# Kernel optimization log

Hardware: AMD Instinct MI355X
Metric: run time of the kernel (lower is better)

## Reference

```python
import jax, jax.numpy as jnp
import numpy as np

NS, NW, E, DIN, OUT, H = 100_000, 400_000, 500_000, 64, 64, 4


def setup_inputs() -> dict:
    key = jax.random.key(0)
    ks = jax.random.split(key, 26)
    s = 1.0 / np.sqrt(DIN)
    sg = 1.0 / np.sqrt(OUT)
    inp = {
        "x_sites": jax.random.normal(ks[0], (NS, DIN), jnp.float32),
        "x_wells": jax.random.normal(ks[1], (NW, DIN), jnp.float32),
        "edge_sw_src": jax.random.randint(ks[2], (E,), 0, NS, jnp.int32),
        "edge_sw_dst": jax.random.randint(ks[3], (E,), 0, NW, jnp.int32),
        "edge_ws_src": jax.random.randint(ks[4], (E,), 0, NW, jnp.int32),
        "edge_ws_dst": jax.random.randint(ks[5], (E,), 0, NS, jnp.int32),
        # GAT ('pfas_sites','distance','gw_wells'), heads=4, concat=False
        "W_sw": jax.random.normal(ks[6], (DIN, H * OUT), jnp.float32) * s,
        "att_src_sw": jax.random.normal(ks[7], (H, OUT), jnp.float32) * sg,
        "att_dst_sw": jax.random.normal(ks[8], (H, OUT), jnp.float32) * sg,
        "b_sw": jnp.zeros((OUT,), jnp.float32),
        # SAGE ('gw_wells','distance','pfas_sites')
        "Wl_ws": jax.random.normal(ks[9], (DIN, OUT), jnp.float32) * s,
        "bl_ws": jnp.zeros((OUT,), jnp.float32),
        "Wr_ws": jax.random.normal(ks[10], (DIN, OUT), jnp.float32) * s,
        # GAT ('pfas_sites','self_loop','pfas_sites'), add_self_loops=True -> identity edges
        "W_ss": jax.random.normal(ks[11], (DIN, H * OUT), jnp.float32) * s,
        "att_src_ss": jax.random.normal(ks[12], (H, OUT), jnp.float32) * sg,
        "att_dst_ss": jax.random.normal(ks[13], (H, OUT), jnp.float32) * sg,
        "b_ss": jnp.zeros((OUT,), jnp.float32),
        # SAGE ('gw_wells','self_loop','gw_wells') with identity edges
        "Wl_ww": jax.random.normal(ks[14], (DIN, OUT), jnp.float32) * s,
        "bl_ww": jnp.zeros((OUT,), jnp.float32),
        "Wr_ww": jax.random.normal(ks[15], (DIN, OUT), jnp.float32) * s,
        # output heads
        "Wg": jax.random.normal(ks[16], (OUT, 1), jnp.float32) * sg,
        "bg": jnp.zeros((1,), jnp.float32),
        "Wsit": jax.random.normal(ks[17], (OUT, 1), jnp.float32) * sg,
        "bsit": jnp.zeros((1,), jnp.float32),
    }
    return inp


def _gat(x_src, x_dst, src, dst, W, a_src, a_dst, b, n_dst):
    """PyG GATConv, concat=False (mean over heads), negative_slope=0.2."""
    h, c = a_src.shape
    xs = (x_src @ W).reshape(-1, h, c)  # [Ns,H,C]
    xd = (x_dst @ W).reshape(-1, h, c)  # [Nd,H,C]
    al_s = jnp.einsum("nhc,hc->nh", xs, a_src)
    al_d = jnp.einsum("nhc,hc->nh", xd, a_dst)
    e = jax.nn.leaky_relu(al_s[src] + al_d[dst], 0.2)  # [E,H]
    m = jax.ops.segment_max(e, dst, num_segments=n_dst)
    ex = jnp.exp(e - m[dst])
    denom = jax.ops.segment_sum(ex, dst, num_segments=n_dst)
    alpha = ex / denom[dst]  # edge-softmax per dst node
    msg = xs[src] * alpha[:, :, None]  # [E,H,C] dominant intermediate
    out = jax.ops.segment_sum(msg, dst, num_segments=n_dst)
    return out.mean(axis=1) + b


def _sage(x_src, x_dst, src, dst, Wl, bl, Wr, n_dst):
    """PyG SAGEConv, mean aggregation, root_weight=True."""
    ssum = jax.ops.segment_sum(x_src[src], dst, num_segments=n_dst)
    cnt = jax.ops.segment_sum(jnp.ones((src.shape[0],), x_src.dtype), dst, num_segments=n_dst)
    mean = ssum / jnp.maximum(cnt, 1.0)[:, None]  # empty neighborhood -> 0 (PyG mean scatter)
    return mean @ Wl + bl + x_dst @ Wr


def reference(x_sites, x_wells, edge_sw_src, edge_sw_dst, edge_ws_src, edge_ws_dst,
              W_sw, att_src_sw, att_dst_sw, b_sw, Wl_ws, bl_ws, Wr_ws,
              W_ss, att_src_ss, att_dst_ss, b_ss, Wl_ww, bl_ww, Wr_ww,
              Wg, bg, Wsit, bsit):
    # relation 1: GAT sites -> wells
    gw = _gat(x_sites, x_wells, edge_sw_src, edge_sw_dst, W_sw, att_src_sw, att_dst_sw, b_sw, NW)
    # relation 4: SAGE self-loop on wells; identity edges -> mean == x itself
    gw = gw + (x_wells @ Wl_ww + bl_ww + x_wells @ Wr_ww)  # HeteroConv aggr='sum'
    # relation 2: SAGE wells -> sites
    si = _sage(x_wells, x_sites, edge_ws_src, edge_ws_dst, Wl_ws, bl_ws, Wr_ws, NS)
    # relation 3: GAT self-loop on sites (add_self_loops=True -> identity edge set);
    # softmax over a single self edge is 1, so output = mean over heads of lin(x) + bias
    si = si + (x_sites @ W_ss).reshape(NS, H, OUT).mean(axis=1) + b_ss
    # post: relu -> dropout (eval mode: identity) -> linear -> leaky_relu(0.01)
    gw = jax.nn.relu(gw)
    si = jax.nn.relu(si)
    o_gw = jax.nn.leaky_relu(gw @ Wg + bg, 0.01)   # [NW, 1]
    o_si = jax.nn.leaky_relu(si @ Wsit + bsit, 0.01)  # [NS, 1]
    return o_gw, o_si
```

## Files before the change

kernel.cpp:

```cpp
#include <hip/hip_runtime.h>

#define NS_ 100000
#define NW_ 400000
#define NE_ 500000
#define EPB 2048

typedef float f32x4_t __attribute__((ext_vector_type(4)));
typedef unsigned u32x4_t __attribute__((ext_vector_type(4)));

__device__ __forceinline__ float lrelu02(float x) { return x > 0.f ? x : 0.2f * x; }
__device__ __forceinline__ float bf2f(unsigned short u) {
    return __uint_as_float(((unsigned)u) << 16);
}
__device__ __forceinline__ unsigned short f2bf(float f) {
    unsigned u = __float_as_uint(f);
    u += 0x7FFFu + ((u >> 16) & 1u);
    return (unsigned short)(u >> 16);
}
__device__ __forceinline__ unsigned pk(float lo, float hi) {
    return (unsigned)f2bf(lo) | ((unsigned)f2bf(hi) << 16);
}
__device__ __forceinline__ void mfma_bf16(f32x4_t& acc, u32x4_t a, u32x4_t b) {
    asm volatile("v_mfma_f32_16x16x32_bf16 %0, %1, %2, %0" : "+v"(acc) : "v"(a), "v"(b));
}

__global__ void __launch_bounds__(256)
k_prep(const float* __restrict__ W_sw, const float* __restrict__ att_src,
       const float* __restrict__ att_dst,
       const float* __restrict__ Wl_ww, const float* __restrict__ Wr_ww,
       const float* __restrict__ Wl_ws, const float* __restrict__ Wr_ws,
       const float* __restrict__ W_ss,
       float* __restrict__ vd, float* __restrict__ vs,
       u32x4_t* __restrict__ fw, u32x4_t* __restrict__ fs,
       u32x4_t* __restrict__ fgw)
{
    const int tid = threadIdx.x;
    {
        int d = tid >> 2, h = tid & 3;
        const float4* wp = (const float4*)(W_sw + d * 256 + h * 64);
        const float4* ad = (const float4*)(att_dst + h * 64);
        const float4* as = (const float4*)(att_src + h * 64);
        float accd = 0.f, accs = 0.f;
#pragma unroll
        for (int c = 0; c < 16; ++c) {
            float4 wv = wp[c]; float4 dv = ad[c]; float4 sv = as[c];
            accd += wv.x * dv.x + wv.y * dv.y + wv.z * dv.z + wv.w * dv.w;
            accs += wv.x * sv.x + wv.y * sv.y + wv.z * sv.z + wv.w * sv.w;
        }
        vd[d * 4 + h] = accd;
        vs[d * 4 + h] = accs;
    }
    for (int idx = tid; idx < 512; idx += 256) {
        int f = idx >> 6, lane = idx & 63;
        int kc = f >> 2, ct = f & 3, q = lane >> 4, n = lane & 15;
        int c = ct * 16 + n;
        u32x4_t d;
#pragma unroll
        for (int i = 0; i < 4; ++i) {
            int k = kc * 32 + q * 8 + 2 * i;
            d[i] = pk(Wl_ww[k * 64 + c] + Wr_ww[k * 64 + c],
                      Wl_ww[(k + 1) * 64 + c] + Wr_ww[(k + 1) * 64 + c]);
        }
        fw[idx] = d;
    }
    for (int idx = tid; idx < 1024; idx += 256) {
        int f = idx >> 6, lane = idx & 63;
        int kc = f >> 2, ct = f & 3, q = lane >> 4, n = lane & 15;
        int c = ct * 16 + n;
        u32x4_t d;
#pragma unroll
        for (int i = 0; i < 4; ++i) {
            int k = kc * 32 + q * 8 + 2 * i;
            float lo, hi;
            if (k < 64) {
                lo = Wl_ws[k * 64 + c];
                hi = Wl_ws[(k + 1) * 64 + c];
            } else {
                int kk = k - 64;
                lo = Wr_ws[kk * 64 + c] + 0.25f * (W_ss[kk * 256 + c] + W_ss[kk * 256 + 64 + c] +
                                                   W_ss[kk * 256 + 128 + c] + W_ss[kk * 256 + 192 + c]);
                hi = Wr_ws[(kk + 1) * 64 + c] + 0.25f * (W_ss[(kk + 1) * 256 + c] + W_ss[(kk + 1) * 256 + 64 + c] +
                                                         W_ss[(kk + 1) * 256 + 128 + c] + W_ss[(kk + 1) * 256 + 192 + c]);
            }
            d[i] = pk(lo, hi);
        }
        fs[idx] = d;
    }
    for (int idx = tid; idx < 2048; idx += 256) {
        int f = idx >> 6, lane = idx & 63;
        int kc = f >> 2, ct = f & 3, q = lane >> 4, n = lane & 15;
        int c = ct * 16 + n;
        u32x4_t d;
#pragma unroll
        for (int i = 0; i < 4; ++i) {
            int kk = kc * 32 + q * 8 + 2 * i;
            int h = kk >> 6, k0 = kk & 63;
            d[i] = pk(W_sw[k0 * 256 + h * 64 + c], W_sw[(k0 + 1) * 256 + h * 64 + c]);
        }
        fgw[idx] = d;
    }
}

__global__ void __launch_bounds__(256)
k_sites_al(const float* __restrict__ x_sites, const float* __restrict__ vs,
           unsigned short* __restrict__ xbf, float* __restrict__ al_s)
{
    __shared__ float vsl[256];
    const int tid = threadIdx.x;
    vsl[tid] = vs[tid];
    __syncthreads();
    const int s = blockIdx.x * 64 + (tid >> 2);
    const int qq = tid & 3;
    if (s >= NS_) return;
    const float* xr = x_sites + (size_t)s * 64 + qq * 16;
    float4 a = *(const float4*)(xr);
    float4 b = *(const float4*)(xr + 4);
    float4 c = *(const float4*)(xr + 8);
    float4 d = *(const float4*)(xr + 12);
    float pa[4];
#pragma unroll
    for (int h = 0; h < 4; ++h) {
        const float* v = &vsl[(qq * 16) * 4 + h];
        pa[h] = a.x * v[0]  + a.y * v[4]  + a.z * v[8]  + a.w * v[12]
              + b.x * v[16] + b.y * v[20] + b.z * v[24] + b.w * v[28]
              + c.x * v[32] + c.y * v[36] + c.z * v[40] + c.w * v[44]
              + d.x * v[48] + d.y * v[52] + d.z * v[56] + d.w * v[60];
    }
#pragma unroll
    for (int h = 0; h < 4; ++h) {
        pa[h] += __shfl_xor(pa[h], 1, 64);
        pa[h] += __shfl_xor(pa[h], 2, 64);
    }
    if (qq == 0)
        *(float4*)(al_s + (size_t)s * 4) = make_float4(pa[0], pa[1], pa[2], pa[3]);
    u32x4_t lo = { pk(a.x, a.y), pk(a.z, a.w), pk(b.x, b.y), pk(b.z, b.w) };
    u32x4_t hi = { pk(c.x, c.y), pk(c.z, c.w), pk(d.x, d.y), pk(d.z, d.w) };
    unsigned short* xo = xbf + (size_t)s * 64 + qq * 16;
    *(u32x4_t*)(xo) = lo;
    *(u32x4_t*)(xo + 8) = hi;
}

__global__ void __launch_bounds__(256)
k_hist2(const int* __restrict__ d1, int* __restrict__ h1,
        const int* __restrict__ d2, int* __restrict__ h2)
{
    int e = blockIdx.x * 256 + threadIdx.x;
    if (e >= NE_) return;
    if (blockIdx.y == 0) atomicAdd(&h1[d1[e]], 1);
    else                 atomicAdd(&h2[d2[e]], 1);
}

__global__ void __launch_bounds__(256)
k_scan1_2(const int* __restrict__ h1, int n1, int* __restrict__ b1, int nb1,
          const int* __restrict__ h2, int n2, int* __restrict__ b2)
{
    __shared__ int red[256];
    const int tid = threadIdx.x;
    const int bx = blockIdx.x;
    const int* hist; int n; int* bsum; int blk;
    if (bx < nb1) { hist = h1; n = n1; bsum = b1; blk = bx; }
    else          { hist = h2; n = n2; bsum = b2; blk = bx - nb1; }
    int base = blk * EPB + tid * 8;
    int s = 0;
#pragma unroll
    for (int i = 0; i < 8; ++i) { int idx = base + i; if (idx < n) s += hist[idx]; }
    red[tid] = s;
    __syncthreads();
    for (int off = 128; off > 0; off >>= 1) {
        if (tid < off) red[tid] += red[tid + off];
        __syncthreads();
    }
    if (tid == 0) bsum[blk] = red[0];
}

__global__ void __launch_bounds__(256)
k_scan2_2(int* __restrict__ b1, int nb1, int* __restrict__ b2, int nb2)
{
    __shared__ int sh[256];
    const int tid = threadIdx.x;
    int* bsum = blockIdx.x == 0 ? b1 : b2;
    int nb = blockIdx.x == 0 ? nb1 : nb2;
    sh[tid] = (tid < nb) ? bsum[tid] : 0;
    __syncthreads();
    for (int off = 1; off < 256; off <<= 1) {
        int u = (tid >= off) ? sh[tid - off] : 0;
        __syncthreads();
        sh[tid] += u;
        __syncthreads();
    }
    if (tid < nb) bsum[tid] = (tid == 0) ? 0 : sh[tid - 1];
}

__global__ void __launch_bounds__(256)
k_scan3_2(const int* __restrict__ h1, int n1, const int* __restrict__ b1,
          int* __restrict__ rp1, int* __restrict__ cu1, int nb1,
          const int* __restrict__ h2, int n2, const int* __restrict__ b2,
          int* __restrict__ rp2, int* __restrict__ cu2)
{
    __shared__ int tsum[256];
    const int tid = threadIdx.x;
    const int bx = blockIdx.x;
    const int* hist; int n; const int* bsum; int* rowptr; int* cursor; int blk;
    if (bx < nb1) { hist = h1; n = n1; bsum = b1; rowptr = rp1; cursor = cu1; blk = bx; }
    else          { hist = h2; n = n2; bsum = b2; rowptr = rp2; cursor = cu2; blk = bx - nb1; }
    int base = blk * EPB + tid * 8;
    int v[8]; int s = 0;
#pragma unroll
    for (int i = 0; i < 8; ++i) {
        int idx = base + i;
        v[i] = (idx < n) ? hist[idx] : 0;
        s += v[i];
    }
    tsum[tid] = s;
    __syncthreads();
    for (int off = 1; off < 256; off <<= 1) {
        int u = (tid >= off) ? tsum[tid - off] : 0;
        __syncthreads();
        tsum[tid] += u;
        __syncthreads();
    }
    int texcl = tsum[tid] - s;
    int run = bsum[blk] + texcl;
#pragma unroll
    for (int i = 0; i < 8; ++i) {
        int idx = base + i;
        if (idx < n) { rowptr[idx] = run; cursor[idx] = run; run += v[i]; }
    }
    if (blk == 0 && tid == 0) rowptr[n] = NE_;
}

__global__ void __launch_bounds__(256)
k_scatter2(const int* __restrict__ s1, const int* __restrict__ d1,
           int* __restrict__ c1, int* __restrict__ o1,
           const int* __restrict__ s2, const int* __restrict__ d2,
           int* __restrict__ c2, int* __restrict__ o2)
{
    int e = blockIdx.x * 256 + threadIdx.x;
    if (e >= NE_) return;
    if (blockIdx.y == 0) { int p = atomicAdd(&c1[d1[e]], 1); o1[p] = s1[e]; }
    else                 { int p = atomicAdd(&c2[d2[e]], 1); o2[p] = s2[e]; }
}

__global__ void __launch_bounds__(256)
k_gat_wells(const float* __restrict__ x_wells, const float* __restrict__ vd,
            const int* __restrict__ rowptr, const int* __restrict__ csr_src,
            const float* __restrict__ al_s, const unsigned short* __restrict__ xbf,
            const float* __restrict__ b_sw, const float* __restrict__ bl_ww,
            const u32x4_t* __restrict__ fw, const u32x4_t* __restrict__ fgw,
            const float* __restrict__ Wg, const float* __restrict__ bg,
            float* __restrict__ out)
{
    __shared__ float vdl[16][17];
    __shared__ unsigned xwB[16][36];
    __shared__ unsigned agB[16][132];
    __shared__ float dl[16][68];
    __shared__ float biasl[64];
    __shared__ float wgl[64];
    __shared__ float res[16];
    const int tid = threadIdx.x;
    vdl[tid >> 4][tid & 15] = vd[tid];
    if (tid < 64) { biasl[tid] = b_sw[tid] + bl_ww[tid]; wgl[tid] = Wg[tid]; }
    __syncthreads();
    const int wl = tid >> 4, p = tid & 15;
    const int w = blockIdx.x * 16 + wl;
    float h0, h1, h2, h3;
    {
        float4 xv = *(const float4*)(x_wells + (size_t)w * 64 + 4 * p);
        *(uint2*)&xwB[wl][2 * p] = make_uint2(pk(xv.x, xv.y), pk(xv.z, xv.w));
        const float* vp = vdl[p];
        h0 = xv.x * vp[0] + xv.y * vp[4] + xv.z * vp[8]  + xv.w * vp[12];
        h1 = xv.x * vp[1] + xv.y * vp[5] + xv.z * vp[9]  + xv.w * vp[13];
        h2 = xv.x * vp[2] + xv.y * vp[6] + xv.z * vp[10] + xv.w * vp[14];
        h3 = xv.x * vp[3] + xv.y * vp[7] + xv.z * vp[11] + xv.w * vp[15];
    }
#pragma unroll
    for (int off = 1; off < 16; off <<= 1) {
        h0 += __shfl_xor(h0, off, 64);
        h1 += __shfl_xor(h1, off, 64);
        h2 += __shfl_xor(h2, off, 64);
        h3 += __shfl_xor(h3, off, 64);
    }
    const int r0 = rowptr[w], r1 = rowptr[w + 1];
    float den0 = 0, den1 = 0, den2 = 0, den3 = 0;
    float a00=0,a01=0,a02=0,a03=0, a10=0,a11=0,a12=0,a13=0;
    float a20=0,a21=0,a22=0,a23=0, a30=0,a31=0,a32=0,a33=0;
    for (int j = r0; j < r1; ++j) {
        int s = csr_src[j];
        float4 as = ((const float4*)al_s)[s];
        ushort4 u = *(const ushort4*)(xbf + (size_t)s * 64 + 4 * p);
        float e0 = __expf(lrelu02(as.x + h0));
        float e1 = __expf(lrelu02(as.y + h1));
        float e2 = __expf(lrelu02(as.z + h2));
        float e3 = __expf(lrelu02(as.w + h3));
        den0 += e0; den1 += e1; den2 += e2; den3 += e3;
        float x0 = bf2f(u.x), x1 = bf2f(u.y), x2 = bf2f(u.z), x3 = bf2f(u.w);
        a00 += e0 * x0; a01 += e0 * x1; a02 += e0 * x2; a03 += e0 * x3;
        a10 += e1 * x0; a11 += e1 * x1; a12 += e1 * x2; a13 += e1 * x3;
        a20 += e2 * x0; a21 += e2 * x1; a22 += e2 * x2; a23 += e2 * x3;
        a30 += e3 * x0; a31 += e3 * x1; a32 += e3 * x2; a33 += e3 * x3;
    }
    if (r1 > r0) {
        float i0 = 0.25f / den0, i1 = 0.25f / den1, i2 = 0.25f / den2, i3 = 0.25f / den3;
        a00 *= i0; a01 *= i0; a02 *= i0; a03 *= i0;
        a10 *= i1; a11 *= i1; a12 *= i1; a13 *= i1;
        a20 *= i2; a21 *= i2; a22 *= i2; a23 *= i2;
        a30 *= i3; a31 *= i3; a32 *= i3; a33 *= i3;
    }
    *(uint2*)&agB[wl][0 * 32 + 2 * p] = make_uint2(pk(a00, a01), pk(a02, a03));
    *(uint2*)&agB[wl][1 * 32 + 2 * p] = make_uint2(pk(a10, a11), pk(a12, a13));
    *(uint2*)&agB[wl][2 * 32 + 2 * p] = make_uint2(pk(a20, a21), pk(a22, a23));
    *(uint2*)&agB[wl][3 * 32 + 2 * p] = make_uint2(pk(a30, a31), pk(a32, a33));
    __syncthreads();
    const int wave = __builtin_amdgcn_readfirstlane(tid >> 6);
    const int lane = tid & 63, q = lane >> 4, n = lane & 15;
    u32x4_t ax0 = *(const u32x4_t*)&xwB[n][q * 4];
    u32x4_t ax1 = *(const u32x4_t*)&xwB[n][16 + q * 4];
    f32x4_t acc = {0, 0, 0, 0};
    asm volatile("s_nop 3" : "+v"(ax0), "+v"(ax1), "+v"(acc));
    mfma_bf16(acc, ax0, fw[wave * 64 + lane]);
    mfma_bf16(acc, ax1, fw[(4 + wave) * 64 + lane]);
#pragma unroll
    for (int kc = 0; kc < 8; ++kc) {
        u32x4_t a = *(const u32x4_t*)&agB[n][kc * 16 + q * 4];
        mfma_bf16(acc, a, fgw[(kc * 4 + wave) * 64 + lane]);
    }
    asm volatile("s_nop 7\n\ts_nop 7" : "+v"(acc));
#pragma unroll
    for (int reg = 0; reg < 4; ++reg)
        dl[q * 4 + reg][wave * 16 + n] = acc[reg];
    __syncthreads();
    const int c0 = 4 * p;
    float4 dv = *(const float4*)&dl[wl][c0];
    float t0 = dv.x + biasl[c0];
    float t1 = dv.y + biasl[c0 + 1];
    float t2 = dv.z + biasl[c0 + 2];
    float t3 = dv.w + biasl[c0 + 3];
    float pr = fmaxf(t0, 0.f) * wgl[c0] + fmaxf(t1, 0.f) * wgl[c0 + 1] +
               fmaxf(t2, 0.f) * wgl[c0 + 2] + fmaxf(t3, 0.f) * wgl[c0 + 3];
    pr += __shfl_xor(pr, 1, 64);
    pr += __shfl_xor(pr, 2, 64);
    pr += __shfl_xor(pr, 4, 64);
    pr += __shfl_xor(pr, 8, 64);
    if (p == 0) res[wl] = pr + bg[0];
    __syncthreads();
    if (tid < 16) {
        float v = res[tid];
        out[blockIdx.x * 16 + tid] = v > 0.f ? v : 0.01f * v;
    }
}

__global__ void __launch_bounds__(256)
k_sage_sites(const float* __restrict__ x_sites, const float* __restrict__ x_wells,
             const int* __restrict__ rowptr, const int* __restrict__ csr_src,
             const u32x4_t* __restrict__ fs, const float* __restrict__ bl_ws,
             const float* __restrict__ b_ss, const float* __restrict__ Wsit,
             const float* __restrict__ bsit, float* __restrict__ out)
{
    __shared__ unsigned mnB[16][36];
    __shared__ unsigned xB[16][36];
    __shared__ float dl[16][68];
    __shared__ float biasl[64];
    __shared__ float wsl[64];
    __shared__ float res[16];
    const int tid = threadIdx.x;
    if (tid < 64) { biasl[tid] = bl_ws[tid] + b_ss[tid]; wsl[tid] = Wsit[tid]; }
    const int sl = tid >> 4, p = tid & 15;
    const int s = blockIdx.x * 16 + sl;
    const int r0 = rowptr[s], r1 = rowptr[s + 1];
    float4 m4 = {0.f, 0.f, 0.f, 0.f};
    for (int j = r0; j < r1; ++j) {
        int wsrc = csr_src[j];
        float4 xv = ((const float4*)(x_wells + (size_t)wsrc * 64))[p];
        m4.x += xv.x; m4.y += xv.y; m4.z += xv.z; m4.w += xv.w;
    }
    if (r1 > r0) {
        float rc = 1.f / (float)(r1 - r0);
        m4.x *= rc; m4.y *= rc; m4.z *= rc; m4.w *= rc;
    }
    *(uint2*)&mnB[sl][2 * p] = make_uint2(pk(m4.x, m4.y), pk(m4.z, m4.w));
    {
        float4 xv = *(const float4*)(x_sites + (size_t)s * 64 + 4 * p);
        *(uint2*)&xB[sl][2 * p] = make_uint2(pk(xv.x, xv.y), pk(xv.z, xv.w));
    }
    __syncthreads();
    const int wave = __builtin_amdgcn_readfirstlane(tid >> 6);
    const int lane = tid & 63, q = lane >> 4, n = lane & 15;
    u32x4_t am0 = *(const u32x4_t*)&mnB[n][q * 4];
    u32x4_t am1 = *(const u32x4_t*)&mnB[n][16 + q * 4];
    u32x4_t ax0 = *(const u32x4_t*)&xB[n][q * 4];
    u32x4_t ax1 = *(const u32x4_t*)&xB[n][16 + q * 4];
    f32x4_t acc = {0, 0, 0, 0};
    asm volatile("s_nop 3" : "+v"(am0), "+v"(am1), "+v"(ax0), "+v"(ax1), "+v"(acc));
    mfma_bf16(acc, am0, fs[wave * 64 + lane]);
    mfma_bf16(acc, am1, fs[(4 + wave) * 64 + lane]);
    mfma_bf16(acc, ax0, fs[(8 + wave) * 64 + lane]);
    mfma_bf16(acc, ax1, fs[(12 + wave) * 64 + lane]);
    asm volatile("s_nop 7\n\ts_nop 7" : "+v"(acc));
#pragma unroll
    for (int reg = 0; reg < 4; ++reg)
        dl[q * 4 + reg][wave * 16 + n] = acc[reg];
    __syncthreads();
    const int c0 = 4 * p;
    float4 dv = *(const float4*)&dl[sl][c0];
    float t0 = dv.x + biasl[c0];
    float t1 = dv.y + biasl[c0 + 1];
    float t2 = dv.z + biasl[c0 + 2];
    float t3 = dv.w + biasl[c0 + 3];
    float pr = fmaxf(t0, 0.f) * wsl[c0] + fmaxf(t1, 0.f) * wsl[c0 + 1] +
               fmaxf(t2, 0.f) * wsl[c0 + 2] + fmaxf(t3, 0.f) * wsl[c0 + 3];
    pr += __shfl_xor(pr, 1, 64);
    pr += __shfl_xor(pr, 2, 64);
    pr += __shfl_xor(pr, 4, 64);
    pr += __shfl_xor(pr, 8, 64);
    if (p == 0) res[sl] = pr + bsit[0];
    __syncthreads();
    if (tid < 16) {
        float v = res[tid];
        out[(size_t)NW_ + blockIdx.x * 16 + tid] = v > 0.f ? v : 0.01f * v;
    }
}

extern "C" void kernel_launch(void* const* d_in, const int* in_sizes, int n_in,
                              void* d_out, int out_size, void* d_ws, size_t ws_size,
                              hipStream_t stream)
{
    const float* x_sites    = (const float*)d_in[0];
    const float* x_wells    = (const float*)d_in[1];
    const int*   e_sw_src   = (const int*)d_in[2];
    const int*   e_sw_dst   = (const int*)d_in[3];
    const int*   e_ws_src   = (const int*)d_in[4];
    const int*   e_ws_dst   = (const int*)d_in[5];
    const float* W_sw       = (const float*)d_in[6];
    const float* att_src_sw = (const float*)d_in[7];
    const float* att_dst_sw = (const float*)d_in[8];
    const float* b_sw       = (const float*)d_in[9];
    const float* Wl_ws      = (const float*)d_in[10];
    const float* bl_ws      = (const float*)d_in[11];
    const float* Wr_ws      = (const float*)d_in[12];
    const float* W_ss       = (const float*)d_in[13];
    const float* b_ss       = (const float*)d_in[16];
    const float* Wl_ww      = (const float*)d_in[17];
    const float* bl_ww      = (const float*)d_in[18];
    const float* Wr_ww      = (const float*)d_in[19];
    const float* Wg         = (const float*)d_in[20];
    const float* bg         = (const float*)d_in[21];
    const float* Wsit       = (const float*)d_in[22];
    const float* bsit       = (const float*)d_in[23];
    float* out = (float*)d_out;

    unsigned short* xbf = (unsigned short*)d_ws;
    float* al_s = (float*)(xbf + (size_t)NS_ * 64);
    float* vd   = al_s + (size_t)NS_ * 4;
    float* vs   = vd + 256;
    u32x4_t* fw = (u32x4_t*)(vs + 256);
    u32x4_t* fs = fw + 512;
    u32x4_t* fgw= fs + 1024;
    int* ip     = (int*)(fgw + 2048);
    int* h_sw   = ip;
    int* h_ws   = h_sw + NW_;
    int* rp_sw  = h_ws + NS_;
    int* cur_sw = rp_sw + NW_ + 4;
    int* csr_sw = cur_sw + NW_;
    int* bs_sw  = csr_sw + NE_;
    int* rp_ws  = bs_sw + 256;
    int* cur_ws = rp_ws + NS_ + 4;
    int* csr_ws = cur_ws + NS_;
    int* bs_ws  = csr_ws + NE_;

    hipMemsetAsync(h_sw, 0, (size_t)(NW_ + NS_) * sizeof(int), stream);

    const int egrid = (NE_ + 255) / 256;
    const int nb_sw = (NW_ + EPB - 1) / EPB;
    const int nb_ws = (NS_ + EPB - 1) / EPB;

    hipLaunchKernelGGL(k_hist2, dim3(egrid, 2), dim3(256), 0, stream,
                       e_sw_dst, h_sw, e_ws_dst, h_ws);
    hipLaunchKernelGGL(k_scan1_2, dim3(nb_sw + nb_ws), dim3(256), 0, stream,
                       h_sw, NW_, bs_sw, nb_sw, h_ws, NS_, bs_ws);
    hipLaunchKernelGGL(k_scan2_2, dim3(2), dim3(256), 0, stream,
                       bs_sw, nb_sw, bs_ws, nb_ws);
    hipLaunchKernelGGL(k_scan3_2, dim3(nb_sw + nb_ws), dim3(256), 0, stream,
                       h_sw, NW_, bs_sw, rp_sw, cur_sw, nb_sw,
                       h_ws, NS_, bs_ws, rp_ws, cur_ws);
    hipLaunchKernelGGL(k_scatter2, dim3(egrid, 2), dim3(256), 0, stream,
                       e_sw_src, e_sw_dst, cur_sw, csr_sw,
                       e_ws_src, e_ws_dst, cur_ws, csr_ws);

    hipLaunchKernelGGL(k_prep, dim3(1), dim3(256), 0, stream,
                       W_sw, att_src_sw, att_dst_sw, Wl_ww, Wr_ww, Wl_ws, Wr_ws, W_ss,
                       vd, vs, fw, fs, fgw);
    hipLaunchKernelGGL(k_sites_al, dim3((NS_ + 63) / 64), dim3(256), 0, stream,
                       x_sites, vs, xbf, al_s);

    hipLaunchKernelGGL(k_gat_wells, dim3(NW_ / 16), dim3(256), 0, stream,
                       x_wells, vd, rp_sw, csr_sw, al_s, xbf, b_sw, bl_ww,
                       fw, fgw, Wg, bg, out);
    hipLaunchKernelGGL(k_sage_sites, dim3(NS_ / 16), dim3(256), 0, stream,
                       x_sites, x_wells, rp_ws, csr_ws, fs, bl_ws, b_ss,
                       Wsit, bsit, out);
}
```

Baseline: 464.7 us.

## Fuse GAT-wells and SAGE-sites into one interleaved kernel, parallelize prep

```diff
diff --git a/kernel.cpp b/kernel.cpp
--- a/kernel.cpp
+++ b/kernel.cpp
@@ -4,6 +4,9 @@
 #define NW_ 400000
 #define NE_ 500000
 #define EPB 2048
+
+#define SAGE_BLKS (NS_ / 16)
+#define GAT_BLKS  (NW_ / 16)
 
 typedef float f32x4_t __attribute__((ext_vector_type(4)));
 typedef unsigned u32x4_t __attribute__((ext_vector_type(4)));
@@ -35,7 +38,8 @@
        u32x4_t* __restrict__ fgw)
 {
     const int tid = threadIdx.x;
-    {
+    const int bid = blockIdx.x;
+    if (bid == 0) {
         int d = tid >> 2, h = tid & 3;
         const float4* wp = (const float4*)(W_sw + d * 256 + h * 64);
         const float4* ad = (const float4*)(att_dst + h * 64);
@@ -49,8 +53,8 @@
         }
         vd[d * 4 + h] = accd;
         vs[d * 4 + h] = accs;
-    }
-    for (int idx = tid; idx < 512; idx += 256) {
+    } else if (bid <= 2) {
+        int idx = (bid - 1) * 256 + tid;
         int f = idx >> 6, lane = idx & 63;
         int kc = f >> 2, ct = f & 3, q = lane >> 4, n = lane & 15;
         int c = ct * 16 + n;
@@ -62,8 +66,8 @@
                       Wl_ww[(k + 1) * 64 + c] + Wr_ww[(k + 1) * 64 + c]);
         }
         fw[idx] = d;
-    }
-    for (int idx = tid; idx < 1024; idx += 256) {
+    } else if (bid <= 6) {
+        int idx = (bid - 3) * 256 + tid;
         int f = idx >> 6, lane = idx & 63;
         int kc = f >> 2, ct = f & 3, q = lane >> 4, n = lane & 15;
         int c = ct * 16 + n;
@@ -85,8 +89,8 @@
             d[i] = pk(lo, hi);
         }
         fs[idx] = d;
-    }
-    for (int idx = tid; idx < 2048; idx += 256) {
+    } else {
+        int idx = (bid - 7) * 256 + tid;
         int f = idx >> 6, lane = idx & 63;
         int kc = f >> 2, ct = f & 3, q = lane >> 4, n = lane & 15;
         int c = ct * 16 + n;
@@ -242,181 +246,201 @@
 }
 
 __global__ void __launch_bounds__(256)
-k_gat_wells(const float* __restrict__ x_wells, const float* __restrict__ vd,
-            const int* __restrict__ rowptr, const int* __restrict__ csr_src,
-            const float* __restrict__ al_s, const unsigned short* __restrict__ xbf,
-            const float* __restrict__ b_sw, const float* __restrict__ bl_ww,
-            const u32x4_t* __restrict__ fw, const u32x4_t* __restrict__ fgw,
-            const float* __restrict__ Wg, const float* __restrict__ bg,
-            float* __restrict__ out)
-{
-    __shared__ float vdl[16][17];
-    __shared__ unsigned xwB[16][36];
-    __shared__ unsigned agB[16][132];
-    __shared__ float dl[16][68];
-    __shared__ float biasl[64];
-    __shared__ float wgl[64];
-    __shared__ float res[16];
+k_fin(const float* __restrict__ x_sites, const float* __restrict__ x_wells,
+      const int* __restrict__ rp_ws, const int* __restrict__ csr_ws,
+      const u32x4_t* __restrict__ fs, const float* __restrict__ bl_ws,
+      const float* __restrict__ b_ss, const float* __restrict__ Wsit,
+      const float* __restrict__ bsit,
+      const float* __restrict__ vd, const int* __restrict__ rp_sw,
+      const int* __restrict__ csr_sw, const float* __restrict__ al_s,
+      const unsigned short* __restrict__ xbf, const float* __restrict__ b_sw,
+      const float* __restrict__ bl_ww, const u32x4_t* __restrict__ fw,
+      const u32x4_t* __restrict__ fgw, const float* __restrict__ Wg,
+      const float* __restrict__ bg, float* __restrict__ out)
+{
+    __shared__ float smem[4192];
     const int tid = threadIdx.x;
-    vdl[tid >> 4][tid & 15] = vd[tid];
-    if (tid < 64) { biasl[tid] = b_sw[tid] + bl_ww[tid]; wgl[tid] = Wg[tid]; }
-    __syncthreads();
-    const int wl = tid >> 4, p = tid & 15;
-    const int w = blockIdx.x * 16 + wl;
-    float h0, h1, h2, h3;
+    const int bid = blockIdx.x;
+
+    if (bid % 5 == 0) {
+        const int sb = bid / 5;
+        unsigned* mnB = (unsigned*)smem;
+        unsigned* xB  = (unsigned*)(smem + 576);
+        float* dl     = smem + 1152;
+        float* biasl  = smem + 2240;
+        float* wsl    = smem + 2304;
+        float* res    = smem + 2368;
+        if (tid < 64) { biasl[tid] = bl_ws[tid] + b_ss[tid]; wsl[tid] = Wsit[tid]; }
+        const int sl = tid >> 4, p = tid & 15;
+        const int s = sb * 16 + sl;
+        const int r0 = rp_ws[s], r1 = rp_ws[s + 1];
+        float4 m4 = {0.f, 0.f, 0.f, 0.f};
+        for (int j = r0; j < r1; ++j) {
+            int wsrc = csr_ws[j];
+            float4 xv = ((const float4*)(x_wells + (size_t)wsrc * 64))[p];
+            m4.x += xv.x; m4.y += xv.y; m4.z += xv.z; m4.w += xv.w;
+        }
+        if (r1 > r0) {
+            float rc = 1.f / (float)(r1 - r0);
+            m4.x *= rc; m4.y *= rc; m4.z *= rc; m4.w *= rc;
+        }
+        {
+            const int c0s = (2 * p + 8 * sl) & 31;
+            mnB[sl * 36 + c0s]     = pk(m4.x, m4.y);
+            mnB[sl * 36 + c0s + 1] = pk(m4.z, m4.w);
+            float4 xv = *(const float4*)(x_sites + (size_t)s * 64 + 4 * p);
+            xB[sl * 36 + c0s]     = pk(xv.x, xv.y);
+            xB[sl * 36 + c0s + 1] = pk(xv.z, xv.w);
+        }
+        __syncthreads();
+        const int wave = __builtin_amdgcn_readfirstlane(tid >> 6);
+        const int lane = tid & 63, q = lane >> 4, n = lane & 15;
+        const int b0 = (4 * q + 8 * n) & 31;
+        const int b1 = (16 + 4 * q + 8 * n) & 31;
+        u32x4_t am0 = *(const u32x4_t*)&mnB[n * 36 + b0];
+        u32x4_t am1 = *(const u32x4_t*)&mnB[n * 36 + b1];
+        u32x4_t ax0 = *(const u32x4_t*)&xB[n * 36 + b0];
+        u32x4_t ax1 = *(const u32x4_t*)&xB[n * 36 + b1];
+        f32x4_t acc = {0, 0, 0, 0};
+        asm volatile("s_nop 3" : "+v"(am0), "+v"(am1), "+v"(ax0), "+v"(ax1), "+v"(acc));
+        mfma_bf16(acc, am0, fs[wave * 64 + lane]);
+        mfma_bf16(acc, am1, fs[(4 + wave) * 64 + lane]);
+        mfma_bf16(acc, ax0, fs[(8 + wave) * 64 + lane]);
+        mfma_bf16(acc, ax1, fs[(12 + wave) * 64 + lane]);
+        asm volatile("s_nop 7\n\ts_nop 7" : "+v"(acc));
+#pragma unroll
+        for (int reg = 0; reg < 4; ++reg)
+            dl[(q * 4 + reg) * 68 + wave * 16 + n] = acc[reg];
+        __syncthreads();
+        const int c0 = 4 * p;
+        float4 dv = *(const float4*)&dl[sl * 68 + c0];
+        float t0 = dv.x + biasl[c0];
+        float t1 = dv.y + biasl[c0 + 1];
+        float t2 = dv.z + biasl[c0 + 2];
+        float t3 = dv.w + biasl[c0 + 3];
+        float pr = fmaxf(t0, 0.f) * wsl[c0] + fmaxf(t1, 0.f) * wsl[c0 + 1] +
+                   fmaxf(t2, 0.f) * wsl[c0 + 2] + fmaxf(t3, 0.f) * wsl[c0 + 3];
+        pr += __shfl_xor(pr, 1, 64);
+        pr += __shfl_xor(pr, 2, 64);
+        pr += __shfl_xor(pr, 4, 64);
+        pr += __shfl_xor(pr, 8, 64);
+        if (p == 0) res[sl] = pr + bsit[0];
+        __syncthreads();
+        if (tid < 16) {
+            float v = res[tid];
+            out[(size_t)NW_ + sb * 16 + tid] = v > 0.f ? v : 0.01f * v;
+        }
+        return;
+    }
+
     {
-        float4 xv = *(const float4*)(x_wells + (size_t)w * 64 + 4 * p);
-        *(uint2*)&xwB[wl][2 * p] = make_uint2(pk(xv.x, xv.y), pk(xv.z, xv.w));
-        const float* vp = vdl[p];
-        h0 = xv.x * vp[0] + xv.y * vp[4] + xv.z * vp[8]  + xv.w * vp[12];
-        h1 = xv.x * vp[1] + xv.y * vp[5] + xv.z * vp[9]  + xv.w * vp[13];
-        h2 = xv.x * vp[2] + xv.y * vp[6] + xv.z * vp[10] + xv.w * vp[14];
-        h3 = xv.x * vp[3] + xv.y * vp[7] + xv.z * vp[11] + xv.w * vp[15];
-    }
-#pragma unroll
-    for (int off = 1; off < 16; off <<= 1) {
-        h0 += __shfl_xor(h0, off, 64);
-        h1 += __shfl_xor(h1, off, 64);
-        h2 += __shfl_xor(h2, off, 64);
-        h3 += __shfl_xor(h3, off, 64);
-    }
-    const int r0 = rowptr[w], r1 = rowptr[w + 1];
-    float den0 = 0, den1 = 0, den2 = 0, den3 = 0;
-    float a00=0,a01=0,a02=0,a03=0, a10=0,a11=0,a12=0,a13=0;
-    float a20=0,a21=0,a22=0,a23=0, a30=0,a31=0,a32=0,a33=0;
-    for (int j = r0; j < r1; ++j) {
-        int s = csr_src[j];
-        float4 as = ((const float4*)al_s)[s];
-        ushort4 u = *(const ushort4*)(xbf + (size_t)s * 64 + 4 * p);
-        float e0 = __expf(lrelu02(as.x + h0));
-        float e1 = __expf(lrelu02(as.y + h1));
-        float e2 = __expf(lrelu02(as.z + h2));
-        float e3 = __expf(lrelu02(as.w + h3));
-        den0 += e0; den1 += e1; den2 += e2; den3 += e3;
-        float x0 = bf2f(u.x), x1 = bf2f(u.y), x2 = bf2f(u.z), x3 = bf2f(u.w);
-        a00 += e0 * x0; a01 += e0 * x1; a02 += e0 * x2; a03 += e0 * x3;
-        a10 += e1 * x0; a11 += e1 * x1; a12 += e1 * x2; a13 += e1 * x3;
-        a20 += e2 * x0; a21 += e2 * x1; a22 += e2 * x2; a23 += e2 * x3;
-        a30 += e3 * x0; a31 += e3 * x1; a32 += e3 * x2; a33 += e3 * x3;
-    }
-    if (r1 > r0) {
-        float i0 = 0.25f / den0, i1 = 0.25f / den1, i2 = 0.25f / den2, i3 = 0.25f / den3;
-        a00 *= i0; a01 *= i0; a02 *= i0; a03 *= i0;
-        a10 *= i1; a11 *= i1; a12 *= i1; a13 *= i1;
-        a20 *= i2; a21 *= i2; a22 *= i2; a23 *= i2;
-        a30 *= i3; a31 *= i3; a32 *= i3; a33 *= i3;
-    }
-    *(uint2*)&agB[wl][0 * 32 + 2 * p] = make_uint2(pk(a00, a01), pk(a02, a03));
-    *(uint2*)&agB[wl][1 * 32 + 2 * p] = make_uint2(pk(a10, a11), pk(a12, a13));
-    *(uint2*)&agB[wl][2 * 32 + 2 * p] = make_uint2(pk(a20, a21), pk(a22, a23));
-    *(uint2*)&agB[wl][3 * 32 + 2 * p] = make_uint2(pk(a30, a31), pk(a32, a33));
-    __syncthreads();
-    const int wave = __builtin_amdgcn_readfirstlane(tid >> 6);
-    const int lane = tid & 63, q = lane >> 4, n = lane & 15;
-    u32x4_t ax0 = *(const u32x4_t*)&xwB[n][q * 4];
-    u32x4_t ax1 = *(const u32x4_t*)&xwB[n][16 + q * 4];
-    f32x4_t acc = {0, 0, 0, 0};
-    asm volatile("s_nop 3" : "+v"(ax0), "+v"(ax1), "+v"(acc));
-    mfma_bf16(acc, ax0, fw[wave * 64 + lane]);
-    mfma_bf16(acc, ax1, fw[(4 + wave) * 64 + lane]);
-#pragma unroll
-    for (int kc = 0; kc < 8; ++kc) {
-        u32x4_t a = *(const u32x4_t*)&agB[n][kc * 16 + q * 4];
-        mfma_bf16(acc, a, fgw[(kc * 4 + wave) * 64 + lane]);
-    }
-    asm volatile("s_nop 7\n\ts_nop 7" : "+v"(acc));
-#pragma unroll
-    for (int reg = 0; reg < 4; ++reg)
-        dl[q * 4 + reg][wave * 16 + n] = acc[reg];
-    __syncthreads();
-    const int c0 = 4 * p;
-    float4 dv = *(const float4*)&dl[wl][c0];
-    float t0 = dv.x + biasl[c0];
-    float t1 = dv.y + biasl[c0 + 1];
-    float t2 = dv.z + biasl[c0 + 2];
-    float t3 = dv.w + biasl[c0 + 3];
-    float pr = fmaxf(t0, 0.f) * wgl[c0] + fmaxf(t1, 0.f) * wgl[c0 + 1] +
-               fmaxf(t2, 0.f) * wgl[c0 + 2] + fmaxf(t3, 0.f) * wgl[c0 + 3];
-    pr += __shfl_xor(pr, 1, 64);
-    pr += __shfl_xor(pr, 2, 64);
-    pr += __shfl_xor(pr, 4, 64);
-    pr += __shfl_xor(pr, 8, 64);
-    if (p == 0) res[wl] = pr + bg[0];
-    __syncthreads();
-    if (tid < 16) {
-        float v = res[tid];
-        out[blockIdx.x * 16 + tid] = v > 0.f ? v : 0.01f * v;
-    }
-}
-
-__global__ void __launch_bounds__(256)
-k_sage_sites(const float* __restrict__ x_sites, const float* __restrict__ x_wells,
-             const int* __restrict__ rowptr, const int* __restrict__ csr_src,
-             const u32x4_t* __restrict__ fs, const float* __restrict__ bl_ws,
-             const float* __restrict__ b_ss, const float* __restrict__ Wsit,
-             const float* __restrict__ bsit, float* __restrict__ out)
-{
-    __shared__ unsigned mnB[16][36];
-    __shared__ unsigned xB[16][36];
-    __shared__ float dl[16][68];
-    __shared__ float biasl[64];
-    __shared__ float wsl[64];
-    __shared__ float res[16];
-    const int tid = threadIdx.x;
-    if (tid < 64) { biasl[tid] = bl_ws[tid] + b_ss[tid]; wsl[tid] = Wsit[tid]; }
-    const int sl = tid >> 4, p = tid & 15;
-    const int s = blockIdx.x * 16 + sl;
-    const int r0 = rowptr[s], r1 = rowptr[s + 1];
-    float4 m4 = {0.f, 0.f, 0.f, 0.f};
-    for (int j = r0; j < r1; ++j) {
-        int wsrc = csr_src[j];
-        float4 xv = ((const float4*)(x_wells + (size_t)wsrc * 64))[p];
-        m4.x += xv.x; m4.y += xv.y; m4.z += xv.z; m4.w += xv.w;
-    }
-    if (r1 > r0) {
-        float rc = 1.f / (float)(r1 - r0);
-        m4.x *= rc; m4.y *= rc; m4.z *= rc; m4.w *= rc;
-    }
-    *(uint2*)&mnB[sl][2 * p] = make_uint2(pk(m4.x, m4.y), pk(m4.z, m4.w));
-    {
-        float4 xv = *(const float4*)(x_sites + (size_t)s * 64 + 4 * p);
-        *(uint2*)&xB[sl][2 * p] = make_uint2(pk(xv.x, xv.y), pk(xv.z, xv.w));
-    }
-    __syncthreads();
-    const int wave = __builtin_amdgcn_readfirstlane(tid >> 6);
-    const int lane = tid & 63, q = lane >> 4, n = lane & 15;
-    u32x4_t am0 = *(const u32x4_t*)&mnB[n][q * 4];
-    u32x4_t am1 = *(const u32x4_t*)&mnB[n][16 + q * 4];
-    u32x4_t ax0 = *(const u32x4_t*)&xB[n][q * 4];
-    u32x4_t ax1 = *(const u32x4_t*)&xB[n][16 + q * 4];
-    f32x4_t acc = {0, 0, 0, 0};
-    asm volatile("s_nop 3" : "+v"(am0), "+v"(am1), "+v"(ax0), "+v"(ax1), "+v"(acc));
-    mfma_bf16(acc, am0, fs[wave * 64 + lane]);
-    mfma_bf16(acc, am1, fs[(4 + wave) * 64 + lane]);
-    mfma_bf16(acc, ax0, fs[(8 + wave) * 64 + lane]);
-    mfma_bf16(acc, ax1, fs[(12 + wave) * 64 + lane]);
-    asm volatile("s_nop 7\n\ts_nop 7" : "+v"(acc));
-#pragma unroll
-    for (int reg = 0; reg < 4; ++reg)
-        dl[q * 4 + reg][wave * 16 + n] = acc[reg];
-    __syncthreads();
-    const int c0 = 4 * p;
-    float4 dv = *(const float4*)&dl[sl][c0];
-    float t0 = dv.x + biasl[c0];
-    float t1 = dv.y + biasl[c0 + 1];
-    float t2 = dv.z + biasl[c0 + 2];
-    float t3 = dv.w + biasl[c0 + 3];
-    float pr = fmaxf(t0, 0.f) * wsl[c0] + fmaxf(t1, 0.f) * wsl[c0 + 1] +
-               fmaxf(t2, 0.f) * wsl[c0 + 2] + fmaxf(t3, 0.f) * wsl[c0 + 3];
-    pr += __shfl_xor(pr, 1, 64);
-    pr += __shfl_xor(pr, 2, 64);
-    pr += __shfl_xor(pr, 4, 64);
-    pr += __shfl_xor(pr, 8, 64);
-    if (p == 0) res[sl] = pr + bsit[0];
-    __syncthreads();
-    if (tid < 16) {
-        float v = res[tid];
-        out[(size_t)NW_ + blockIdx.x * 16 + tid] = v > 0.f ? v : 0.01f * v;
+        const int gb = bid - 1 - bid / 5;
+        float* vdl    = smem;
+        unsigned* xwB = (unsigned*)(smem + 272);
+        unsigned* agB = (unsigned*)(smem + 848);
+        float* dl     = smem + 2960;
+        float* biasl  = smem + 4048;
+        float* wgl    = smem + 4112;
+        float* res    = smem + 4176;
+        vdl[(tid >> 4) * 17 + (tid & 15)] = vd[tid];
+        if (tid < 64) { biasl[tid] = b_sw[tid] + bl_ww[tid]; wgl[tid] = Wg[tid]; }
+        __syncthreads();
+        const int wl = tid >> 4, p = tid & 15;
+        const int w = gb * 16 + wl;
+        const int r0 = rp_sw[w], r1 = rp_sw[w + 1];
+        const int c0w = (2 * p + 8 * wl) & 31;
+        float h0, h1, h2, h3;
+        {
+            float4 xv = *(const float4*)(x_wells + (size_t)w * 64 + 4 * p);
+            xwB[wl * 36 + c0w]     = pk(xv.x, xv.y);
+            xwB[wl * 36 + c0w + 1] = pk(xv.z, xv.w);
+            const float* vp = &vdl[p * 17];
+            h0 = xv.x * vp[0] + xv.y * vp[4] + xv.z * vp[8]  + xv.w * vp[12];
+            h1 = xv.x * vp[1] + xv.y * vp[5] + xv.z * vp[9]  + xv.w * vp[13];
+            h2 = xv.x * vp[2] + xv.y * vp[6] + xv.z * vp[10] + xv.w * vp[14];
+            h3 = xv.x * vp[3] + xv.y * vp[7] + xv.z * vp[11] + xv.w * vp[15];
+        }
+#pragma unroll
+        for (int off = 1; off < 16; off <<= 1) {
+            h0 += __shfl_xor(h0, off, 64);
+            h1 += __shfl_xor(h1, off, 64);
+            h2 += __shfl_xor(h2, off, 64);
+            h3 += __shfl_xor(h3, off, 64);
+        }
+        float den0 = 0, den1 = 0, den2 = 0, den3 = 0;
+        float a00=0,a01=0,a02=0,a03=0, a10=0,a11=0,a12=0,a13=0;
+        float a20=0,a21=0,a22=0,a23=0, a30=0,a31=0,a32=0,a33=0;
+        for (int j = r0; j < r1; ++j) {
+            int s = csr_sw[j];
+            float4 as = ((const float4*)al_s)[s];
+            ushort4 u = *(const ushort4*)(xbf + (size_t)s * 64 + 4 * p);
+            float e0 = __expf(lrelu02(as.x + h0));
+            float e1 = __expf(lrelu02(as.y + h1));
+            float e2 = __expf(lrelu02(as.z + h2));
+            float e3 = __expf(lrelu02(as.w + h3));
+            den0 += e0; den1 += e1; den2 += e2; den3 += e3;
+            float x0 = bf2f(u.x), x1 = bf2f(u.y), x2 = bf2f(u.z), x3 = bf2f(u.w);
+            a00 += e0 * x0; a01 += e0 * x1; a02 += e0 * x2; a03 += e0 * x3;
+            a10 += e1 * x0; a11 += e1 * x1; a12 += e1 * x2; a13 += e1 * x3;
+            a20 += e2 * x0; a21 += e2 * x1; a22 += e2 * x2; a23 += e2 * x3;
+            a30 += e3 * x0; a31 += e3 * x1; a32 += e3 * x2; a33 += e3 * x3;
+        }
+        if (r1 > r0) {
+            float i0 = 0.25f / den0, i1 = 0.25f / den1, i2 = 0.25f / den2, i3 = 0.25f / den3;
+            a00 *= i0; a01 *= i0; a02 *= i0; a03 *= i0;
+            a10 *= i1; a11 *= i1; a12 *= i1; a13 *= i1;
+            a20 *= i2; a21 *= i2; a22 *= i2; a23 *= i2;
+            a30 *= i3; a31 *= i3; a32 *= i3; a33 *= i3;
+        }
+        agB[wl * 132 + 0 * 32 + c0w]     = pk(a00, a01);
+        agB[wl * 132 + 0 * 32 + c0w + 1] = pk(a02, a03);
+        agB[wl * 132 + 1 * 32 + c0w]     = pk(a10, a11);
+        agB[wl * 132 + 1 * 32 + c0w + 1] = pk(a12, a13);
+        agB[wl * 132 + 2 * 32 + c0w]     = pk(a20, a21);
+        agB[wl * 132 + 2 * 32 + c0w + 1] = pk(a22, a23);
+        agB[wl * 132 + 3 * 32 + c0w]     = pk(a30, a31);
+        agB[wl * 132 + 3 * 32 + c0w + 1] = pk(a32, a33);
+        __syncthreads();
+        const int wave = __builtin_amdgcn_readfirstlane(tid >> 6);
+        const int lane = tid & 63, q = lane >> 4, n = lane & 15;
+        const int b0 = (4 * q + 8 * n) & 31;
+        const int b1 = (16 + 4 * q + 8 * n) & 31;
+        u32x4_t ax0 = *(const u32x4_t*)&xwB[n * 36 + b0];
+        u32x4_t ax1 = *(const u32x4_t*)&xwB[n * 36 + b1];
+        f32x4_t acc = {0, 0, 0, 0};
+        asm volatile("s_nop 3" : "+v"(ax0), "+v"(ax1), "+v"(acc));
+        mfma_bf16(acc, ax0, fw[wave * 64 + lane]);
+        mfma_bf16(acc, ax1, fw[(4 + wave) * 64 + lane]);
+#pragma unroll
+        for (int kc = 0; kc < 8; ++kc) {
+            const int hh = kc >> 1;
+            const int sofs = (((kc & 1) * 16) + 4 * q + 8 * n) & 31;
+            u32x4_t a = *(const u32x4_t*)&agB[n * 132 + hh * 32 + sofs];
+            mfma_bf16(acc, a, fgw[(kc * 4 + wave) * 64 + lane]);
+        }
+        asm volatile("s_nop 7\n\ts_nop 7" : "+v"(acc));
+#pragma unroll
+        for (int reg = 0; reg < 4; ++reg)
+            dl[(q * 4 + reg) * 68 + wave * 16 + n] = acc[reg];
+        __syncthreads();
+        const int c0 = 4 * p;
+        float4 dv = *(const float4*)&dl[wl * 68 + c0];
+        float t0 = dv.x + biasl[c0];
+        float t1 = dv.y + biasl[c0 + 1];
+        float t2 = dv.z + biasl[c0 + 2];
+        float t3 = dv.w + biasl[c0 + 3];
+        float pr = fmaxf(t0, 0.f) * wgl[c0] + fmaxf(t1, 0.f) * wgl[c0 + 1] +
+                   fmaxf(t2, 0.f) * wgl[c0 + 2] + fmaxf(t3, 0.f) * wgl[c0 + 3];
+        pr += __shfl_xor(pr, 1, 64);
+        pr += __shfl_xor(pr, 2, 64);
+        pr += __shfl_xor(pr, 4, 64);
+        pr += __shfl_xor(pr, 8, 64);
+        if (p == 0) res[wl] = pr + bg[0];
+        __syncthreads();
+        if (tid < 16) {
+            float v = res[tid];
+            out[gb * 16 + tid] = v > 0.f ? v : 0.01f * v;
+        }
     }
 }
 
@@ -473,6 +497,10 @@
     const int nb_sw = (NW_ + EPB - 1) / EPB;
     const int nb_ws = (NS_ + EPB - 1) / EPB;
 
+    hipLaunchKernelGGL(k_prep, dim3(15), dim3(256), 0, stream,
+                       W_sw, att_src_sw, att_dst_sw, Wl_ww, Wr_ww, Wl_ws, Wr_ws, W_ss,
+                       vd, vs, fw, fs, fgw);
+
     hipLaunchKernelGGL(k_hist2, dim3(egrid, 2), dim3(256), 0, stream,
                        e_sw_dst, h_sw, e_ws_dst, h_ws);
     hipLaunchKernelGGL(k_scan1_2, dim3(nb_sw + nb_ws), dim3(256), 0, stream,
@@ -486,16 +514,11 @@
                        e_sw_src, e_sw_dst, cur_sw, csr_sw,
                        e_ws_src, e_ws_dst, cur_ws, csr_ws);
 
-    hipLaunchKernelGGL(k_prep, dim3(1), dim3(256), 0, stream,
-                       W_sw, att_src_sw, att_dst_sw, Wl_ww, Wr_ww, Wl_ws, Wr_ws, W_ss,
-                       vd, vs, fw, fs, fgw);
     hipLaunchKernelGGL(k_sites_al, dim3((NS_ + 63) / 64), dim3(256), 0, stream,
                        x_sites, vs, xbf, al_s);
 
-    hipLaunchKernelGGL(k_gat_wells, dim3(NW_ / 16), dim3(256), 0, stream,
-                       x_wells, vd, rp_sw, csr_sw, al_s, xbf, b_sw, bl_ww,
-                       fw, fgw, Wg, bg, out);
-    hipLaunchKernelGGL(k_sage_sites, dim3(NS_ / 16), dim3(256), 0, stream,
-                       x_sites, x_wells, rp_ws, csr_ws, fs, bl_ws, b_ss,
-                       Wsit, bsit, out);
-}
+    hipLaunchKernelGGL(k_fin, dim3(SAGE_BLKS + GAT_BLKS), dim3(256), 0, stream,
+                       x_sites, x_wells, rp_ws, csr_ws, fs, bl_ws, b_ss, Wsit, bsit,
+                       vd, rp_sw, csr_sw, al_s, xbf, b_sw, bl_ww, fw, fgw,
+                       Wg, bg, out);
+}
```

Result: faster. 452.3 us (-2.7%).
